# Optimization experiments

Measured on AMD Instinct MI355X. Metric: run time of the kernel, lower is better.

## Reference

```python
import jax, jax.numpy as jnp
import numpy as np

N, L, D = 8192, 50, 64          # nodes, max history length, embed_dim
NUM_USERS = 100000
NUM_ITEMS = 100000
NUM_RATINGS = 5


def setup_inputs() -> dict:
    key = jax.random.key(0)
    ks = jax.random.split(key, 12)
    g = lambda k, shp, s=0.05: jax.random.normal(k, shp, jnp.float32) * s
    return {
        "nodes": jax.random.randint(ks[0], (N,), 0, NUM_USERS),
        "history_uv": jax.random.randint(ks[1], (N, L), 0, NUM_ITEMS),
        "history_r": jax.random.randint(ks[2], (N, L), 0, NUM_RATINGS),
        "hist_len": jax.random.randint(ks[3], (N,), 1, L + 1),  # ragged lengths in [1, L]
        # embedding tables (v2e / u2e / r2e)
        "v2e": g(ks[4], (NUM_ITEMS, D), 0.1),
        "u2e": g(ks[5], (NUM_USERS, D), 0.1),
        "r2e": g(ks[6], (NUM_RATINGS, D), 0.1),
        # w_r1: Dense(2D -> D), w_r2: Dense(D -> D)
        "W1": g(ks[7], (2 * D, D)), "b1": jnp.zeros((D,), jnp.float32),
        "W2": g(ks[8], (D, D)), "b2": jnp.zeros((D,), jnp.float32),
        # Attention MLP: Dense(2D->D), Dense(D->D), Dense(D->1)
        "A1": g(ks[9], (2 * D, D)), "ab1": jnp.zeros((D,), jnp.float32),
        "A2": g(ks[10], (D, D)), "ab2": jnp.zeros((D,), jnp.float32),
        "A3": g(ks[11], (D, 1)), "ab3": jnp.zeros((1,), jnp.float32),
    }


def reference(nodes, history_uv, history_r, hist_len, v2e, u2e, r2e,
              W1, b1, W2, b2, A1, ab1, A2, ab2, A3, ab3):
    # Vectorized form of the per-node Python loop: pad histories to L, mask.
    e_uv = v2e[history_uv]                       # [N,L,D] neighbor item embeds
    uv_rep = u2e[nodes]                          # [N,D]   self (user) embed
    e_r = r2e[history_r]                         # [N,L,D] rating embeds
    x = jnp.concatenate([e_uv, e_r], axis=-1)    # [N,L,2D]
    x = jax.nn.relu(x @ W1 + b1)                 # w_r1 + relu
    o = jax.nn.relu(x @ W2 + b2)                 # w_r2 + relu -> o_history [N,L,D]
    # attention: concat(o_history, repeated uv_rep) -> 2-layer relu MLP -> scalar
    a_in = jnp.concatenate(
        [o, jnp.broadcast_to(uv_rep[:, None, :], o.shape)], axis=-1)  # [N,L,2D]
    h = jax.nn.relu(a_in @ A1 + ab1)
    h = jax.nn.relu(h @ A2 + ab2)
    s = (h @ A3 + ab3)[..., 0]                   # [N,L] attention logits
    mask = jnp.arange(L)[None, :] < hist_len[:, None]
    att = jax.nn.softmax(jnp.where(mask, s, -1e9), axis=-1)  # softmax over history
    # att_history = o_history^T @ att_w, per node -> [N,D]
    return jnp.einsum('nl,nld->nd', att, o)
```

## Files before the change

kernel.cpp:

```cpp
#include <hip/hip_runtime.h>
#include <hip/hip_bf16.h>
#include <stdint.h>

typedef short bfx8 __attribute__((ext_vector_type(8)));
typedef float f32x4 __attribute__((ext_vector_type(4)));

#define MFMA16(a, b, c) __builtin_amdgcn_mfma_f32_16x16x32_bf16(a, b, c, 0, 0, 0)
#define STAGE_FENCE() __builtin_amdgcn_sched_barrier(0x77)
#define PIN_FENCE()   __builtin_amdgcn_sched_barrier(0x47)

#define CB_B1  0
#define CB_B2  64
#define CB_AB1 128
#define CB_AB2 192
#define CB_A3  256
#define CB_AB3 320

__device__ __forceinline__ uint32_t pk2(float a, float b) {
    __hip_bfloat162 h = __float22bfloat162_rn(make_float2(a, b));
    union { __hip_bfloat162 h; uint32_t u; } cv; cv.h = h; return cv.u;
}
__device__ __forceinline__ float bflo(uint32_t w) { return __uint_as_float(w << 16); }
__device__ __forceinline__ float bfhi(uint32_t w) { return __uint_as_float(w & 0xFFFF0000u); }

__device__ __forceinline__ bfx8 pack8(const float4 a, const float4 b) {
    union { bfx8 v; uint32_t u[4]; } r;
    r.u[0] = pk2(a.x, a.y); r.u[1] = pk2(a.z, a.w);
    r.u[2] = pk2(b.x, b.y); r.u[3] = pk2(b.z, b.w);
    return r.v;
}
__device__ __forceinline__ bfx8 packr(f32x4 a, f32x4 b) {
    union { bfx8 v; uint32_t u[4]; } r;
    r.u[0] = pk2(fmaxf(a[0], 0.f), fmaxf(a[1], 0.f));
    r.u[1] = pk2(fmaxf(a[2], 0.f), fmaxf(a[3], 0.f));
    r.u[2] = pk2(fmaxf(b[0], 0.f), fmaxf(b[1], 0.f));
    r.u[3] = pk2(fmaxf(b[2], 0.f), fmaxf(b[3], 0.f));
    return r.v;
}
__device__ __forceinline__ float4 ld4(const float* p) { return *(const float4*)p; }

__device__ __forceinline__ int mix4(int row) {
    return (row & 3) | (((row >> 4) & 1) << 2) | (((row >> 3) & 1) << 3);
}
__device__ __forceinline__ int mix3(int row) {
    return (row & 3) | (((row >> 3) & 1) << 2);
}
__device__ __forceinline__ bfx8 ldw4(const uint8_t* base, int row, int c, int g) {
    int chunk = (4 * c + g) ^ mix4(row);
    return *(const bfx8*)(base + row * 256 + chunk * 16);
}
__device__ __forceinline__ bfx8 ldw2(const uint8_t* base, int row, int c, int g) {
    int chunk = ((4 * c + g) ^ mix3(row)) & 7;
    return *(const bfx8*)(base + row * 128 + chunk * 16);
}
template <int CTRL>
__device__ __forceinline__ float dppadd(float x) {
    int y = __builtin_amdgcn_update_dpp(0, __float_as_int(x), CTRL, 0xF, 0xF, false);
    return x + __int_as_float(y);
}
__device__ __forceinline__ float rowsum16(float x) {
    x = dppadd<0xB1>(x);
    x = dppadd<0x4E>(x);
    x = dppadd<0x124>(x);
    x = dppadd<0x128>(x);
    return x;
}

__global__ __launch_bounds__(512, 1) void uvagg_mfma(
    const int* __restrict__ nodes, const int* __restrict__ huv,
    const int* __restrict__ hr, const int* __restrict__ hlen,
    const float* __restrict__ v2e, const float* __restrict__ u2e,
    const float* __restrict__ r2e,
    const float* __restrict__ W1, const float* __restrict__ b1,
    const float* __restrict__ W2, const float* __restrict__ b2,
    const float* __restrict__ A1, const float* __restrict__ ab1,
    const float* __restrict__ A2, const float* __restrict__ ab2,
    const float* __restrict__ A3, const float* __restrict__ ab3f,
    float* __restrict__ out, int N, int L, int nwaves)
{
    __shared__ __align__(16) uint8_t W1s[64 * 256];
    __shared__ __align__(16) uint8_t A1s[64 * 256];
    __shared__ __align__(16) uint8_t W2s[64 * 128];
    __shared__ __align__(16) uint8_t A2s[64 * 128];
    __shared__ __align__(16) float cb[324];

    const int tid = threadIdx.x;
    for (int i = tid; i < 4096; i += 512) {
        int kp = i >> 6, d = i & 63;
        int addr = d * 256 + ((((kp >> 2) ^ mix4(d)) & 15) << 4) + ((kp & 3) << 2);
        *(uint32_t*)(W1s + addr) = pk2(W1[(2 * kp) * 64 + d], W1[(2 * kp + 1) * 64 + d]);
        *(uint32_t*)(A1s + addr) = pk2(A1[(2 * kp) * 64 + d], A1[(2 * kp + 1) * 64 + d]);
    }
    for (int i = tid; i < 2048; i += 512) {
        int kp = i >> 6, d = i & 63;
        int addr = d * 128 + ((((kp >> 2) ^ mix3(d)) & 7) << 4) + ((kp & 3) << 2);
        *(uint32_t*)(W2s + addr) = pk2(W2[(2 * kp) * 64 + d], W2[(2 * kp + 1) * 64 + d]);
        *(uint32_t*)(A2s + addr) = pk2(A2[(2 * kp) * 64 + d], A2[(2 * kp + 1) * 64 + d]);
    }
    for (int i = tid; i < 321; i += 512) {
        if (i < 64)       cb[CB_B1 + i]        = b1[i];
        else if (i < 128) cb[CB_B2 + i - 64]   = b2[i - 64];
        else if (i < 192) cb[CB_AB1 + i - 128] = ab1[i - 128];
        else if (i < 256) cb[CB_AB2 + i - 192] = ab2[i - 192];
        else if (i < 320) cb[CB_A3 + i - 256]  = A3[i - 256];
        else              cb[CB_AB3]           = ab3f[0];
    }
    __syncthreads();

    const int lane = tid & 63;
    const int wid  = tid >> 6;
    const int s    = lane & 15;
    const int g    = lane >> 4;
    const int rs   = 8 * (s >> 2) + (s & 3);
    const float ab3 = cb[CB_AB3];

    for (int node = blockIdx.x * 8 + wid; node < N; node += nwaves) {
        const int hl = __builtin_amdgcn_readfirstlane(min(hlen[node], L));
        const int un = __builtin_amdgcn_readfirstlane(nodes[node]);

        const float* ur = u2e + (size_t)un * 64;
        const bfx8 uf2 = pack8(ld4(ur + 8 * g),      ld4(ur + 8 * g + 4));
        const bfx8 uf3 = pack8(ld4(ur + 32 + 8 * g), ld4(ur + 36 + 8 * g));

        const int idxlane = min(lane, L - 1);
        const int iu_all = huv[(size_t)node * L + idxlane];
        const int ir_all = hr [(size_t)node * L + idxlane];

        f32x4 h1base[4];
        #pragma unroll
        for (int mt = 0; mt < 4; ++mt) {
            const int dof = 4 * (mt & 1) + 32 * (mt >> 1);
            h1base[mt] = *(const f32x4*)(cb + CB_AB1 + 8 * g + dof);
            const int row = rs + dof;
            h1base[mt] = MFMA16(ldw4(A1s, row, 2, g), uf2, h1base[mt]);
            h1base[mt] = MFMA16(ldw4(A1s, row, 3, g), uf3, h1base[mt]);
        }

        float zacc = 0.0f;
        f32x4 accO[4];
        #pragma unroll
        for (int i = 0; i < 4; ++i) accO[i] = f32x4{0.f, 0.f, 0.f, 0.f};

        const int ntile = (hl + 15) >> 4;

        float4 qa0, qa1, qa2, qa3, qb0, qb1, qb2, qb3;
        {
            const int slot0 = min(s, hl - 1);
            const int iu = __shfl(iu_all, slot0, 64);
            const int ir = __shfl(ir_all, slot0, 64);
            const float* vr = v2e + (size_t)iu * 64;
            const float* rr = r2e + (size_t)ir * 64;
            qa0 = ld4(vr + 8 * g);      qa1 = ld4(vr + 8 * g + 4);
            qa2 = ld4(vr + 32 + 8 * g); qa3 = ld4(vr + 36 + 8 * g);
            qb0 = ld4(rr + 8 * g);      qb1 = ld4(rr + 8 * g + 4);
            qb2 = ld4(rr + 32 + 8 * g); qb3 = ld4(rr + 36 + 8 * g);
        }

        for (int tt = 0; tt < ntile; ++tt) {
            const int gslot = tt * 16 + s;
            const bfx8 f0 = pack8(qa0, qa1);
            const bfx8 f1 = pack8(qa2, qa3);
            const bfx8 f2 = pack8(qb0, qb1);
            const bfx8 f3 = pack8(qb2, qb3);

            f32x4 ah[4];
            #pragma unroll
            for (int mt = 0; mt < 4; ++mt) {
                const int dof = 4 * (mt & 1) + 32 * (mt >> 1);
                ah[mt] = *(const f32x4*)(cb + CB_B1 + 8 * g + dof);
                const int row = rs + dof;
                ah[mt] = MFMA16(ldw4(W1s, row, 0, g), f0, ah[mt]);
                ah[mt] = MFMA16(ldw4(W1s, row, 1, g), f1, ah[mt]);
                ah[mt] = MFMA16(ldw4(W1s, row, 2, g), f2, ah[mt]);
                ah[mt] = MFMA16(ldw4(W1s, row, 3, g), f3, ah[mt]);
            }
            const bfx8 x1a = packr(ah[0], ah[1]);
            const bfx8 x1b = packr(ah[2], ah[3]);

            if (tt + 1 < ntile) {
                const int nslot = min(tt * 16 + 16 + s, hl - 1);
                const int niu = __shfl(iu_all, nslot, 64);
                const int nir = __shfl(ir_all, nslot, 64);
                const float* vr = v2e + (size_t)niu * 64;
                const float* rr = r2e + (size_t)nir * 64;
                qa0 = ld4(vr + 8 * g);      qa1 = ld4(vr + 8 * g + 4);
                qa2 = ld4(vr + 32 + 8 * g); qa3 = ld4(vr + 36 + 8 * g);
                qb0 = ld4(rr + 8 * g);      qb1 = ld4(rr + 8 * g + 4);
                qb2 = ld4(rr + 32 + 8 * g); qb3 = ld4(rr + 36 + 8 * g);
            }
            PIN_FENCE();

            f32x4 ao[4];
            #pragma unroll
            for (int mt = 0; mt < 4; ++mt) {
                const int dof = 4 * (mt & 1) + 32 * (mt >> 1);
                ao[mt] = *(const f32x4*)(cb + CB_B2 + 8 * g + dof);
                const int row = rs + dof;
                ao[mt] = MFMA16(ldw2(W2s, row, 0, g), x1a, ao[mt]);
                ao[mt] = MFMA16(ldw2(W2s, row, 1, g), x1b, ao[mt]);
            }
            const bfx8 oa = packr(ao[0], ao[1]);
            const bfx8 ob = packr(ao[2], ao[3]);
            STAGE_FENCE();

            f32x4 h[4];
            #pragma unroll
            for (int mt = 0; mt < 4; ++mt) {
                h[mt] = h1base[mt];
                const int row = rs + 4 * (mt & 1) + 32 * (mt >> 1);
                h[mt] = MFMA16(ldw4(A1s, row, 0, g), oa, h[mt]);
                h[mt] = MFMA16(ldw4(A1s, row, 1, g), ob, h[mt]);
            }
            const bfx8 h1a = packr(h[0], h[1]);
            const bfx8 h1b = packr(h[2], h[3]);
            STAGE_FENCE();

            float part = 0.0f;
            #pragma unroll
            for (int mt = 0; mt < 4; ++mt) {
                const int dof = 4 * (mt & 1) + 32 * (mt >> 1);
                f32x4 h2 = *(const f32x4*)(cb + CB_AB2 + 8 * g + dof);
                const int row = rs + dof;
                h2 = MFMA16(ldw2(A2s, row, 0, g), h1a, h2);
                h2 = MFMA16(ldw2(A2s, row, 1, g), h1b, h2);
                const f32x4 aq = *(const f32x4*)(cb + CB_A3 + 8 * g + dof);
                part = fmaf(fmaxf(h2[0], 0.f), aq[0], part);
                part = fmaf(fmaxf(h2[1], 0.f), aq[1], part);
                part = fmaf(fmaxf(h2[2], 0.f), aq[2], part);
                part = fmaf(fmaxf(h2[3], 0.f), aq[3], part);
            }
            STAGE_FENCE();
            float p2 = part + __shfl_xor(part, 16, 64);
            const float sl = p2 + __shfl_xor(p2, 32, 64) + ab3;
            const float p = (gslot < hl) ? __expf(sl) : 0.0f;
            zacc += p;
            union { bfx8 v; uint32_t u[4]; } ua, ub;
            ua.v = oa; ub.v = ob;
            #pragma unroll
            for (int j = 0; j < 2; ++j) {
                accO[0][2*j+0] = fmaf(p, bflo(ua.u[j]),     accO[0][2*j+0]);
                accO[0][2*j+1] = fmaf(p, bfhi(ua.u[j]),     accO[0][2*j+1]);
                accO[1][2*j+0] = fmaf(p, bflo(ua.u[2 + j]), accO[1][2*j+0]);
                accO[1][2*j+1] = fmaf(p, bfhi(ua.u[2 + j]), accO[1][2*j+1]);
                accO[2][2*j+0] = fmaf(p, bflo(ub.u[j]),     accO[2][2*j+0]);
                accO[2][2*j+1] = fmaf(p, bfhi(ub.u[j]),     accO[2][2*j+1]);
                accO[3][2*j+0] = fmaf(p, bflo(ub.u[2 + j]), accO[3][2*j+0]);
                accO[3][2*j+1] = fmaf(p, bfhi(ub.u[2 + j]), accO[3][2*j+1]);
            }
        }

        const float Z = rowsum16(zacc);
        #pragma unroll
        for (int mt = 0; mt < 4; ++mt)
            #pragma unroll
            for (int r = 0; r < 4; ++r)
                accO[mt][r] = rowsum16(accO[mt][r]);
        const float inv = 1.0f / Z;
        if (s == 0) {
            float* op = out + (size_t)node * 64;
            #pragma unroll
            for (int mt = 0; mt < 4; ++mt) {
                const int dof = 8 * g + 4 * (mt & 1) + 32 * (mt >> 1);
                *(float4*)(op + dof) = make_float4(accO[mt][0] * inv, accO[mt][1] * inv,
                                                   accO[mt][2] * inv, accO[mt][3] * inv);
            }
        }
    }
}

extern "C" void kernel_launch(void* const* d_in, const int* in_sizes, int n_in,
                              void* d_out, int out_size, void* d_ws, size_t ws_size,
                              hipStream_t stream) {
    const int*   nodes = (const int*)d_in[0];
    const int*   huv   = (const int*)d_in[1];
    const int*   hrr   = (const int*)d_in[2];
    const int*   hlen  = (const int*)d_in[3];
    const float* v2e   = (const float*)d_in[4];
    const float* u2e   = (const float*)d_in[5];
    const float* r2e   = (const float*)d_in[6];
    const float* W1    = (const float*)d_in[7];
    const float* b1    = (const float*)d_in[8];
    const float* W2    = (const float*)d_in[9];
    const float* b2    = (const float*)d_in[10];
    const float* A1    = (const float*)d_in[11];
    const float* ab1   = (const float*)d_in[12];
    const float* A2    = (const float*)d_in[13];
    const float* ab2   = (const float*)d_in[14];
    const float* A3    = (const float*)d_in[15];
    const float* ab3   = (const float*)d_in[16];
    float* out = (float*)d_out;

    const int N = in_sizes[0];
    const int L = in_sizes[1] / N;
    int blocks = (N + 7) / 8;
    if (blocks > 512) blocks = 512;
    const int nwaves = blocks * 8;

    hipLaunchKernelGGL(uvagg_mfma, dim3(blocks), dim3(512), 0, stream,
                       nodes, huv, hrr, hlen, v2e, u2e, r2e,
                       W1, b1, W2, b2, A1, ab1, A2, ab2, A3, ab3,
                       out, N, L, nwaves);
}
```

Before: 48.46 us.

## Use atomic work queue for node scheduling and precompute swizzled LDS addresses

Replaces the static grid-stride assignment of nodes to waves with a global atomic counter, so each wave grabs its next node dynamically. This is meant to balance the ragged history lengths across waves. It also merges the shared-memory weight buffers into one buffer and precomputes per-lane swizzled base pointers, which removes the per-load XOR address arithmetic. The cost is one atomic per node, plus an extra memset launch to reset the counter in the workspace.

```diff
diff --git a/kernel.cpp b/kernel.cpp
--- a/kernel.cpp
+++ b/kernel.cpp
@@ -9,12 +9,16 @@
 #define STAGE_FENCE() __builtin_amdgcn_sched_barrier(0x77)
 #define PIN_FENCE()   __builtin_amdgcn_sched_barrier(0x47)
 
-#define CB_B1  0
-#define CB_B2  64
-#define CB_AB1 128
-#define CB_AB2 192
-#define CB_A3  256
-#define CB_AB3 320
+#define OFF_W1 0
+#define OFF_A1 16384
+#define OFF_W2 32768
+#define OFF_A2 40960
+#define OFF_CB 49152
+#define CBB_B1  0
+#define CBB_B2  256
+#define CBB_AB1 512
+#define CBB_AB2 768
+#define CBB_A3  1024
 
 __device__ __forceinline__ uint32_t pk2(float a, float b) {
     __hip_bfloat162 h = __float22bfloat162_rn(make_float2(a, b));
@@ -44,14 +48,6 @@
 }
 __device__ __forceinline__ int mix3(int row) {
     return (row & 3) | (((row >> 3) & 1) << 2);
-}
-__device__ __forceinline__ bfx8 ldw4(const uint8_t* base, int row, int c, int g) {
-    int chunk = (4 * c + g) ^ mix4(row);
-    return *(const bfx8*)(base + row * 256 + chunk * 16);
-}
-__device__ __forceinline__ bfx8 ldw2(const uint8_t* base, int row, int c, int g) {
-    int chunk = ((4 * c + g) ^ mix3(row)) & 7;
-    return *(const bfx8*)(base + row * 128 + chunk * 16);
 }
 template <int CTRL>
 __device__ __forceinline__ float dppadd(float x) {
@@ -76,45 +72,59 @@
     const float* __restrict__ A1, const float* __restrict__ ab1,
     const float* __restrict__ A2, const float* __restrict__ ab2,
     const float* __restrict__ A3, const float* __restrict__ ab3f,
-    float* __restrict__ out, int N, int L, int nwaves)
+    float* __restrict__ out, int N, int L, int* __restrict__ cnt)
 {
-    __shared__ __align__(16) uint8_t W1s[64 * 256];
-    __shared__ __align__(16) uint8_t A1s[64 * 256];
-    __shared__ __align__(16) uint8_t W2s[64 * 128];
-    __shared__ __align__(16) uint8_t A2s[64 * 128];
-    __shared__ __align__(16) float cb[324];
+    __shared__ __align__(16) uint8_t smem[50448];
+    float* cbf = (float*)(smem + OFF_CB);
 
     const int tid = threadIdx.x;
     for (int i = tid; i < 4096; i += 512) {
         int kp = i >> 6, d = i & 63;
         int addr = d * 256 + ((((kp >> 2) ^ mix4(d)) & 15) << 4) + ((kp & 3) << 2);
-        *(uint32_t*)(W1s + addr) = pk2(W1[(2 * kp) * 64 + d], W1[(2 * kp + 1) * 64 + d]);
-        *(uint32_t*)(A1s + addr) = pk2(A1[(2 * kp) * 64 + d], A1[(2 * kp + 1) * 64 + d]);
+        *(uint32_t*)(smem + OFF_W1 + addr) = pk2(W1[(2 * kp) * 64 + d], W1[(2 * kp + 1) * 64 + d]);
+        *(uint32_t*)(smem + OFF_A1 + addr) = pk2(A1[(2 * kp) * 64 + d], A1[(2 * kp + 1) * 64 + d]);
     }
     for (int i = tid; i < 2048; i += 512) {
         int kp = i >> 6, d = i & 63;
         int addr = d * 128 + ((((kp >> 2) ^ mix3(d)) & 7) << 4) + ((kp & 3) << 2);
-        *(uint32_t*)(W2s + addr) = pk2(W2[(2 * kp) * 64 + d], W2[(2 * kp + 1) * 64 + d]);
-        *(uint32_t*)(A2s + addr) = pk2(A2[(2 * kp) * 64 + d], A2[(2 * kp + 1) * 64 + d]);
+        *(uint32_t*)(smem + OFF_W2 + addr) = pk2(W2[(2 * kp) * 64 + d], W2[(2 * kp + 1) * 64 + d]);
+        *(uint32_t*)(smem + OFF_A2 + addr) = pk2(A2[(2 * kp) * 64 + d], A2[(2 * kp + 1) * 64 + d]);
     }
     for (int i = tid; i < 321; i += 512) {
-        if (i < 64)       cb[CB_B1 + i]        = b1[i];
-        else if (i < 128) cb[CB_B2 + i - 64]   = b2[i - 64];
-        else if (i < 192) cb[CB_AB1 + i - 128] = ab1[i - 128];
-        else if (i < 256) cb[CB_AB2 + i - 192] = ab2[i - 192];
-        else if (i < 320) cb[CB_A3 + i - 256]  = A3[i - 256];
-        else              cb[CB_AB3]           = ab3f[0];
+        if (i < 64)       cbf[i]       = b1[i];
+        else if (i < 128) cbf[i]       = b2[i - 64];
+        else if (i < 192) cbf[i]       = ab1[i - 128];
+        else if (i < 256) cbf[i]       = ab2[i - 192];
+        else if (i < 320) cbf[i]       = A3[i - 256];
+        else              cbf[320]     = ab3f[0];
     }
     __syncthreads();
 
     const int lane = tid & 63;
-    const int wid  = tid >> 6;
     const int s    = lane & 15;
     const int g    = lane >> 4;
-    const int rs   = 8 * (s >> 2) + (s & 3);
-    const float ab3 = cb[CB_AB3];
-
-    for (int node = blockIdx.x * 8 + wid; node < N; node += nwaves) {
+    const int r    = s & 3;
+    const int q    = s >> 2;
+    const int rs   = 8 * q + r;
+
+    const int cx = ((q >> 1) | ((q & 1) << 1));
+    const int base1 = rs * 256 + ((g ^ r) << 4) + (cx << 6);
+    const int base2 = rs * 128 + ((g ^ r) << 4) + ((q & 1) << 6);
+    const uint8_t* pw0 = smem + (base1 ^ (0 << 6));
+    const uint8_t* pw1 = smem + (base1 ^ (1 << 6));
+    const uint8_t* pw2 = smem + (base1 ^ (2 << 6));
+    const uint8_t* pw3 = smem + (base1 ^ (3 << 6));
+    const uint8_t* pq0 = smem + (base2 ^ (0 << 6));
+    const uint8_t* pq1 = smem + (base2 ^ (1 << 6));
+    const uint8_t* pcb = smem + OFF_CB + 32 * g;
+    const float ab3 = cbf[320];
+
+    for (;;) {
+        int node0 = 0;
+        if (lane == 0) node0 = atomicAdd(cnt, 1);
+        const int node = __builtin_amdgcn_readfirstlane(node0);
+        if (node >= N) break;
+
         const int hl = __builtin_amdgcn_readfirstlane(min(hlen[node], L));
         const int un = __builtin_amdgcn_readfirstlane(nodes[node]);
 
@@ -130,10 +140,9 @@
         #pragma unroll
         for (int mt = 0; mt < 4; ++mt) {
             const int dof = 4 * (mt & 1) + 32 * (mt >> 1);
-            h1base[mt] = *(const f32x4*)(cb + CB_AB1 + 8 * g + dof);
-            const int row = rs + dof;
-            h1base[mt] = MFMA16(ldw4(A1s, row, 2, g), uf2, h1base[mt]);
-            h1base[mt] = MFMA16(ldw4(A1s, row, 3, g), uf3, h1base[mt]);
+            h1base[mt] = *(const f32x4*)(pcb + CBB_AB1 + dof * 4);
+            h1base[mt] = MFMA16(*(const bfx8*)(pw2 + OFF_A1 + dof * 256), uf2, h1base[mt]);
+            h1base[mt] = MFMA16(*(const bfx8*)(pw3 + OFF_A1 + dof * 256), uf3, h1base[mt]);
         }
 
         float zacc = 0.0f;
@@ -167,12 +176,11 @@
             #pragma unroll
             for (int mt = 0; mt < 4; ++mt) {
                 const int dof = 4 * (mt & 1) + 32 * (mt >> 1);
-                ah[mt] = *(const f32x4*)(cb + CB_B1 + 8 * g + dof);
-                const int row = rs + dof;
-                ah[mt] = MFMA16(ldw4(W1s, row, 0, g), f0, ah[mt]);
-                ah[mt] = MFMA16(ldw4(W1s, row, 1, g), f1, ah[mt]);
-                ah[mt] = MFMA16(ldw4(W1s, row, 2, g), f2, ah[mt]);
-                ah[mt] = MFMA16(ldw4(W1s, row, 3, g), f3, ah[mt]);
+                ah[mt] = *(const f32x4*)(pcb + CBB_B1 + dof * 4);
+                ah[mt] = MFMA16(*(const bfx8*)(pw0 + OFF_W1 + dof * 256), f0, ah[mt]);
+                ah[mt] = MFMA16(*(const bfx8*)(pw1 + OFF_W1 + dof * 256), f1, ah[mt]);
+                ah[mt] = MFMA16(*(const bfx8*)(pw2 + OFF_W1 + dof * 256), f2, ah[mt]);
+                ah[mt] = MFMA16(*(const bfx8*)(pw3 + OFF_W1 + dof * 256), f3, ah[mt]);
             }
             const bfx8 x1a = packr(ah[0], ah[1]);
             const bfx8 x1b = packr(ah[2], ah[3]);
@@ -194,10 +202,9 @@
             #pragma unroll
             for (int mt = 0; mt < 4; ++mt) {
                 const int dof = 4 * (mt & 1) + 32 * (mt >> 1);
-                ao[mt] = *(const f32x4*)(cb + CB_B2 + 8 * g + dof);
-                const int row = rs + dof;
-                ao[mt] = MFMA16(ldw2(W2s, row, 0, g), x1a, ao[mt]);
-                ao[mt] = MFMA16(ldw2(W2s, row, 1, g), x1b, ao[mt]);
+                ao[mt] = *(const f32x4*)(pcb + CBB_B2 + dof * 4);
+                ao[mt] = MFMA16(*(const bfx8*)(pq0 + OFF_W2 + dof * 128), x1a, ao[mt]);
+                ao[mt] = MFMA16(*(const bfx8*)(pq1 + OFF_W2 + dof * 128), x1b, ao[mt]);
             }
             const bfx8 oa = packr(ao[0], ao[1]);
             const bfx8 ob = packr(ao[2], ao[3]);
@@ -206,10 +213,10 @@
             f32x4 h[4];
             #pragma unroll
             for (int mt = 0; mt < 4; ++mt) {
+                const int dof = 4 * (mt & 1) + 32 * (mt >> 1);
                 h[mt] = h1base[mt];
-                const int row = rs + 4 * (mt & 1) + 32 * (mt >> 1);
-                h[mt] = MFMA16(ldw4(A1s, row, 0, g), oa, h[mt]);
-                h[mt] = MFMA16(ldw4(A1s, row, 1, g), ob, h[mt]);
+                h[mt] = MFMA16(*(const bfx8*)(pw0 + OFF_A1 + dof * 256), oa, h[mt]);
+                h[mt] = MFMA16(*(const bfx8*)(pw1 + OFF_A1 + dof * 256), ob, h[mt]);
             }
             const bfx8 h1a = packr(h[0], h[1]);
             const bfx8 h1b = packr(h[2], h[3]);
@@ -219,11 +226,10 @@
             #pragma unroll
             for (int mt = 0; mt < 4; ++mt) {
                 const int dof = 4 * (mt & 1) + 32 * (mt >> 1);
-                f32x4 h2 = *(const f32x4*)(cb + CB_AB2 + 8 * g + dof);
-                const int row = rs + dof;
-                h2 = MFMA16(ldw2(A2s, row, 0, g), h1a, h2);
-                h2 = MFMA16(ldw2(A2s, row, 1, g), h1b, h2);
-                const f32x4 aq = *(const f32x4*)(cb + CB_A3 + 8 * g + dof);
+                f32x4 h2 = *(const f32x4*)(pcb + CBB_AB2 + dof * 4);
+                h2 = MFMA16(*(const bfx8*)(pq0 + OFF_A2 + dof * 128), h1a, h2);
+                h2 = MFMA16(*(const bfx8*)(pq1 + OFF_A2 + dof * 128), h1b, h2);
+                const f32x4 aq = *(const f32x4*)(pcb + CBB_A3 + dof * 4);
                 part = fmaf(fmaxf(h2[0], 0.f), aq[0], part);
                 part = fmaf(fmaxf(h2[1], 0.f), aq[1], part);
                 part = fmaf(fmaxf(h2[2], 0.f), aq[2], part);
@@ -253,8 +259,8 @@
         #pragma unroll
         for (int mt = 0; mt < 4; ++mt)
             #pragma unroll
-            for (int r = 0; r < 4; ++r)
-                accO[mt][r] = rowsum16(accO[mt][r]);
+            for (int rr2 = 0; rr2 < 4; ++rr2)
+                accO[mt][rr2] = rowsum16(accO[mt][rr2]);
         const float inv = 1.0f / Z;
         if (s == 0) {
             float* op = out + (size_t)node * 64;
@@ -292,12 +298,14 @@
 
     const int N = in_sizes[0];
     const int L = in_sizes[1] / N;
+
+    hipMemsetAsync(d_ws, 0, sizeof(int), stream);
+
     int blocks = (N + 7) / 8;
     if (blocks > 512) blocks = 512;
-    const int nwaves = blocks * 8;
 
     hipLaunchKernelGGL(uvagg_mfma, dim3(blocks), dim3(512), 0, stream,
                        nodes, huv, hrr, hlen, v2e, u2e, r2e,
                        W1, b1, W2, b2, A1, ab1, A2, ab2, A3, ab3,
-                       out, N, L, nwaves);
-}
+                       out, N, L, (int*)d_ws);
+}
```

After: 153.4 us. 3.17x slower.
